# Kernel tuning notes

Hardware: AMD Instinct MI355X
Metric: run time of the kernel (lower is better)

Reference implementation:

```python
import jax, jax.numpy as jnp
import numpy as np

NUM_CLASSES = 2
NORM_EPS = 1e-12   # F.normalize default
COS_EPS = 1e-8     # nn.CosineSimilarity default
MEAN_EPS = 1e-6


def _l2_normalize_c(x):
    # normalize over channel dim (dim=1), per (batch, pixel) -- matches
    # F.normalize(x.view(-1,16,256*256), dim=1)
    n = jnp.sqrt(jnp.sum(x * x, axis=1, keepdims=True))
    return x / jnp.maximum(n, NORM_EPS)


def _cos_c(a, b):
    # cosine similarity along channel dim, torch semantics
    dot = jnp.sum(a * b, axis=1)
    na = jnp.sqrt(jnp.sum(a * a, axis=1))
    nb = jnp.sqrt(jnp.sum(b * b, axis=1))
    return dot / jnp.maximum(na * nb, COS_EPS)


def setup_inputs() -> dict:
    key = jax.random.key(0)
    k1, k2, k3 = jax.random.split(key, 3)
    preds_S = jax.random.normal(k1, (32, 16, 256, 256), dtype=jnp.float32)
    preds_T = jax.random.normal(k2, (32, 16, 256, 256), dtype=jnp.float32)
    target = jax.random.randint(k3, (32, 256, 256), 0, NUM_CLASSES, dtype=jnp.int64)
    return {"preds_S": preds_S, "preds_T": preds_T, "target": target}


def reference(preds_S, preds_T, target):
    feat_S = _l2_normalize_c(preds_S)  # [B,16,H,W]
    feat_T = _l2_normalize_c(preds_T)
    # target is already HxW == feature size, so nearest upsample is identity
    tar = target[:, None, :, :].astype(feat_S.dtype)  # [B,1,H,W], broadcasts over C

    center_S, center_T = feat_S, feat_T
    center_S_FS, center_T_FS = feat_S, feat_T
    for i in range(NUM_CLASSES):
        mask = (tar == i).astype(feat_S.dtype)  # [B,1,H,W]
        cnt = jnp.sum(mask, axis=(-2, -1)) + MEAN_EPS  # [B,1]
        mean_S = (jnp.sum(mask * feat_S, axis=(-2, -1)) / cnt)[:, :, None, None]  # [B,16,1,1]
        mean_T = (jnp.sum(mask * feat_T, axis=(-2, -1)) / cnt)[:, :, None, None]
        center_S = (1.0 - mask) * center_S + mask * mean_S
        center_T = (1.0 - mask) * center_T + mask * mean_T
        center_S_FS = mask * center_S_FS + (1.0 - mask) * mean_S
        center_T_FS = mask * center_T_FS + (1.0 - mask) * mean_T

    pcsim_S = jnp.exp(_cos_c(feat_S, center_S) - _cos_c(feat_S, center_S_FS))
    pcsim_T = jnp.exp(_cos_c(feat_T, center_T) - _cos_c(feat_T, center_T_FS))
    return jnp.mean((pcsim_S - pcsim_T) ** 2)
```

## Files before the change

### kernel.cpp

```cpp
#include <hip/hip_runtime.h>
#include <math.h>

#define NBATCH 32
#define NCH 16
#define HW 65536
#define SLICES1 32
#define SLICES2 32
#define TPB 256

#define CT_PART  0
#define CT_N1P   65536
#define CT_LOSSP 66560
#define CT_FLOATS 67584

#define CACHE_HALFS ((size_t)2 * NBATCH * NCH * HW)
#define CACHE_BYTES (CACHE_HALFS * 2)

typedef float f4 __attribute__((ext_vector_type(4)));
typedef _Float16 h4 __attribute__((ext_vector_type(4)));
typedef _Float16 h8 __attribute__((ext_vector_type(8)));

__device__ __forceinline__ float wave_sum(float v) {
#pragma unroll
  for (int off = 32; off > 0; off >>= 1) v += __shfl_down(v, off, 64);
  return v;
}

template <bool CACHE>
__global__ __launch_bounds__(TPB) void k_sums(const float* __restrict__ S,
                                              const float* __restrict__ T,
                                              const int* __restrict__ tgt,
                                              float* __restrict__ ctrl,
                                              _Float16* __restrict__ cache) {
  const int b = blockIdx.y;
  const int slice = blockIdx.x;
  const int which = blockIdx.z;
  const int tid = threadIdx.x;
  const int lane = tid & 63, wid = tid >> 6;

  const float* Xb = (which ? T : S) + (size_t)b * NCH * HW;
  const int* tb = tgt + (size_t)b * HW;
  _Float16* cb = cache + ((size_t)(which * NBATCH + b)) * NCH * HW;

  const int base = slice * (HW / SLICES1) + tid * 4;

  float acc0[NCH], acc1[NCH];
#pragma unroll
  for (int i = 0; i < NCH; ++i) { acc0[i] = 0.f; acc1[i] = 0.f; }
  float n1 = 0.f;

  for (int it = 0; it < 2; ++it) {
    const int p = base + it * (TPB * 4);
    const int4 tv = *(const int4*)(tb + p);
    f4 x[NCH];
#pragma unroll
    for (int i = 0; i < NCH; ++i)
      x[i] = __builtin_nontemporal_load((const f4*)(Xb + (size_t)i * HW + p));

    const float m0 = (tv.x == 1) ? 1.f : 0.f;
    const float m1 = (tv.y == 1) ? 1.f : 0.f;
    const float m2 = (tv.z == 1) ? 1.f : 0.f;
    const float m3 = (tv.w == 1) ? 1.f : 0.f;
    n1 += (m0 + m1) + (m2 + m3);

    float s0a = 0.f, s0b = 0.f, s1a = 0.f, s1b = 0.f;
    float s2a = 0.f, s2b = 0.f, s3a = 0.f, s3b = 0.f;
#pragma unroll
    for (int i = 0; i < NCH; i += 2) {
      s0a = fmaf(x[i].x, x[i].x, s0a);   s0b = fmaf(x[i + 1].x, x[i + 1].x, s0b);
      s1a = fmaf(x[i].y, x[i].y, s1a);   s1b = fmaf(x[i + 1].y, x[i + 1].y, s1b);
      s2a = fmaf(x[i].z, x[i].z, s2a);   s2b = fmaf(x[i + 1].z, x[i + 1].z, s2b);
      s3a = fmaf(x[i].w, x[i].w, s3a);   s3b = fmaf(x[i + 1].w, x[i + 1].w, s3b);
    }
    const float i0 = 1.f / fmaxf(sqrtf(s0a + s0b), 1e-12f);
    const float i1 = 1.f / fmaxf(sqrtf(s1a + s1b), 1e-12f);
    const float i2 = 1.f / fmaxf(sqrtf(s2a + s2b), 1e-12f);
    const float i3 = 1.f / fmaxf(sqrtf(s3a + s3b), 1e-12f);

#pragma unroll
    for (int i = 0; i < NCH; ++i) {
      const float f0 = x[i].x * i0, f1 = x[i].y * i1;
      const float f2 = x[i].z * i2, f3 = x[i].w * i3;
      if constexpr (CACHE) {
        h4 q;
        q.x = (_Float16)f0; q.y = (_Float16)f1;
        q.z = (_Float16)f2; q.w = (_Float16)f3;
        __builtin_nontemporal_store(q, (h4*)(cb + (size_t)i * HW + p));
      }
      const float t_ = (f0 + f1) + (f2 + f3);
      const float m_ = fmaf(f0, m0, fmaf(f1, m1, fmaf(f2, m2, f3 * m3)));
      acc1[i] += m_;
      acc0[i] += t_ - m_;
    }
  }

  __shared__ float lds[32][TPB + 1];
  __shared__ float redn[4];
#pragma unroll
  for (int i = 0; i < NCH; ++i) {
    lds[i][tid] = acc0[i];
    lds[16 + i][tid] = acc1[i];
  }
  n1 = wave_sum(n1);
  if (lane == 0) redn[wid] = n1;
  __syncthreads();

  const int row = tid >> 3, seg = tid & 7;
  float s = 0.f;
#pragma unroll
  for (int k0 = 0; k0 < 32; ++k0) {
    const int k = (k0 + seg * 4) & 31;
    s += lds[row][seg * 32 + k];
  }
  s += __shfl_down(s, 4, 8);
  s += __shfl_down(s, 2, 8);
  s += __shfl_down(s, 1, 8);

  float* part = ctrl + CT_PART + (((size_t)which * NBATCH + b) * SLICES1 + slice) * 32;
  if (seg == 0) part[row] = s;
  if (tid == 0 && which == 0)
    ctrl[CT_N1P + b * SLICES1 + slice] = redn[0] + redn[1] + redn[2] + redn[3];
}

__device__ __forceinline__ float pc_one(float ss, float d0, float d1, int t,
                                        float nm0, float nm1) {
  const float n = sqrtf(ss);
  const float inv = 1.f / fmaxf(n, 1e-12f);
  const float na = n * inv;
  const float c0 = (d0 * inv) / fmaxf(na * nm0, 1e-8f);
  const float c1 = (d1 * inv) / fmaxf(na * nm1, 1e-8f);
  return expf((t == 1) ? (c1 - c0) : (c0 - c1));
}

template <bool CACHE>
__global__ __launch_bounds__(TPB) void k_pass2(const float* __restrict__ S,
                                               const float* __restrict__ T,
                                               const int* __restrict__ tgt,
                                               float* __restrict__ ctrl,
                                               const _Float16* __restrict__ cache) {
  __shared__ __align__(16) float sm[72];
  __shared__ float ldp[4][64];
  __shared__ float ldn[32];
  __shared__ float red4[4];
  const int b = blockIdx.y;
  const int slice = blockIdx.x;
  const int tid = threadIdx.x;

  {
    const int c64 = tid & 63, q = tid >> 6;
    const int t_ = c64 >> 5, c32 = c64 & 31;
    const float* pp = ctrl + CT_PART + (((size_t)t_ * NBATCH + b) * SLICES1) * 32 + c32;
    float s8 = 0.f;
#pragma unroll
    for (int k = 0; k < 8; ++k) s8 += pp[(q * 8 + k) * 32];
    ldp[q][c64] = s8;
  }
  if (tid < 32) ldn[tid] = ctrl[CT_N1P + b * SLICES1 + tid];
  __syncthreads();

  if (tid < 64) {
    float n1 = 0.f;
#pragma unroll
    for (int k = 0; k < 32; ++k) n1 += ldn[k];
    const int cls = (tid >> 4) & 1;
    const float cnt = (cls ? n1 : ((float)HW - n1)) + 1e-6f;
    sm[tid] = (ldp[0][tid] + ldp[1][tid] + ldp[2][tid] + ldp[3][tid]) / cnt;
  }
  __syncthreads();
  if (tid < 4) {
    float ss = 0.f;
    const int base_ = (tid >> 1) * 32 + (tid & 1) * 16;
#pragma unroll
    for (int c = 0; c < NCH; ++c) { const float v = sm[base_ + c]; ss = fmaf(v, v, ss); }
    sm[64 + tid] = sqrtf(ss);
  }
  __syncthreads();

  const int* tb = tgt + (size_t)b * HW;
  float lacc = 0.f;

  if constexpr (CACHE) {
    const _Float16* cS = cache + (size_t)b * NCH * HW;
    const _Float16* cT = cache + ((size_t)(NBATCH + b)) * NCH * HW;
    const float rS0 = 1.f / fmaxf(sm[64], 1e-8f);
    const float rS1 = 1.f / fmaxf(sm[65], 1e-8f);
    const float rT0 = 1.f / fmaxf(sm[66], 1e-8f);
    const float rT1 = 1.f / fmaxf(sm[67], 1e-8f);

    const int p = slice * (HW / SLICES2) + tid * 8;
    const int4 tva = *(const int4*)(tb + p);
    const int4 tvb = *(const int4*)(tb + p + 4);
    const int t8[8] = {tva.x, tva.y, tva.z, tva.w, tvb.x, tvb.y, tvb.z, tvb.w};

    h8 xs[NCH], xt[NCH];
#pragma unroll
    for (int i = 0; i < NCH; ++i)
      xs[i] = __builtin_nontemporal_load((const h8*)(cS + (size_t)i * HW + p));
#pragma unroll
    for (int i = 0; i < NCH; ++i)
      xt[i] = __builtin_nontemporal_load((const h8*)(cT + (size_t)i * HW + p));

    float a0[8], a1[8];
#pragma unroll
    for (int k = 0; k < 8; ++k) { a0[k] = 0.f; a1[k] = 0.f; }
#pragma unroll
    for (int i = 0; i < NCH; ++i) {
      const float w0 = sm[i], w1 = sm[16 + i];
#pragma unroll
      for (int k = 0; k < 8; ++k) {
        const float xv = (float)xs[i][k];
        a0[k] = fmaf(xv, w0, a0[k]);
        a1[k] = fmaf(xv, w1, a1[k]);
      }
    }
    float pcS[8];
#pragma unroll
    for (int k = 0; k < 8; ++k)
      pcS[k] = expf((t8[k] == 1) ? a1[k] * rS1 - a0[k] * rS0
                                 : a0[k] * rS0 - a1[k] * rS1);

#pragma unroll
    for (int k = 0; k < 8; ++k) { a0[k] = 0.f; a1[k] = 0.f; }
#pragma unroll
    for (int i = 0; i < NCH; ++i) {
      const float w0 = sm[32 + i], w1 = sm[48 + i];
#pragma unroll
      for (int k = 0; k < 8; ++k) {
        const float xv = (float)xt[i][k];
        a0[k] = fmaf(xv, w0, a0[k]);
        a1[k] = fmaf(xv, w1, a1[k]);
      }
    }
#pragma unroll
    for (int k = 0; k < 8; ++k) {
      const float pcT = expf((t8[k] == 1) ? a1[k] * rT1 - a0[k] * rT0
                                          : a0[k] * rT0 - a1[k] * rT1);
      const float e = pcS[k] - pcT;
      lacc = fmaf(e, e, lacc);
    }
  } else {
    const float* Sb = S + (size_t)b * NCH * HW;
    const float* Tb = T + (size_t)b * NCH * HW;
    const float nmS0 = sm[64], nmS1 = sm[65], nmT0 = sm[66], nmT1 = sm[67];
    const int base = slice * (HW / SLICES2) + tid * 2;

    for (int it = 0; it < 4; ++it) {
      const int p = base + it * (TPB * 2);
      const int2 tv = *(const int2*)(tb + p);
      float2 xs[NCH], xt[NCH];
#pragma unroll
      for (int i = 0; i < NCH; ++i) xs[i] = *(const float2*)(Sb + (size_t)i * HW + p);
#pragma unroll
      for (int i = 0; i < NCH; ++i) xt[i] = *(const float2*)(Tb + (size_t)i * HW + p);

      float ss0 = 0.f, ss1 = 0.f, d00 = 0.f, d01 = 0.f, d10 = 0.f, d11 = 0.f;
#pragma unroll
      for (int i = 0; i < NCH; ++i) {
        const float w0 = sm[i], w1 = sm[16 + i];
        ss0 = fmaf(xs[i].x, xs[i].x, ss0); ss1 = fmaf(xs[i].y, xs[i].y, ss1);
        d00 = fmaf(xs[i].x, w0, d00);      d01 = fmaf(xs[i].y, w0, d01);
        d10 = fmaf(xs[i].x, w1, d10);      d11 = fmaf(xs[i].y, w1, d11);
      }
      const float pcS0 = pc_one(ss0, d00, d10, tv.x, nmS0, nmS1);
      const float pcS1 = pc_one(ss1, d01, d11, tv.y, nmS0, nmS1);

      ss0 = 0.f; ss1 = 0.f; d00 = 0.f; d01 = 0.f; d10 = 0.f; d11 = 0.f;
#pragma unroll
      for (int i = 0; i < NCH; ++i) {
        const float w0 = sm[32 + i], w1 = sm[48 + i];
        ss0 = fmaf(xt[i].x, xt[i].x, ss0); ss1 = fmaf(xt[i].y, xt[i].y, ss1);
        d00 = fmaf(xt[i].x, w0, d00);      d01 = fmaf(xt[i].y, w0, d01);
        d10 = fmaf(xt[i].x, w1, d10);      d11 = fmaf(xt[i].y, w1, d11);
      }
      const float pcT0 = pc_one(ss0, d00, d10, tv.x, nmT0, nmT1);
      const float pcT1 = pc_one(ss1, d01, d11, tv.y, nmT0, nmT1);

      const float e0 = pcS0 - pcT0, e1 = pcS1 - pcT1;
      lacc += e0 * e0 + e1 * e1;
    }
  }

  lacc = wave_sum(lacc);
  if ((tid & 63) == 0) red4[tid >> 6] = lacc;
  __syncthreads();
  if (tid == 0)
    ctrl[CT_LOSSP + b * SLICES2 + slice] = red4[0] + red4[1] + red4[2] + red4[3];
}

__global__ void k_final(const float* __restrict__ ctrl, float* __restrict__ out) {
  __shared__ float r4[4];
  const int tid = threadIdx.x;
  float s = ctrl[CT_LOSSP + tid] + ctrl[CT_LOSSP + tid + 256] +
            ctrl[CT_LOSSP + tid + 512] + ctrl[CT_LOSSP + tid + 768];
  s = wave_sum(s);
  if ((tid & 63) == 0) r4[tid >> 6] = s;
  __syncthreads();
  if (tid == 0)
    out[0] = (r4[0] + r4[1] + r4[2] + r4[3]) * (1.f / 2097152.f);
}

extern "C" void kernel_launch(void* const* d_in, const int* in_sizes, int n_in,
                              void* d_out, int out_size, void* d_ws, size_t ws_size,
                              hipStream_t stream) {
  const float* S = (const float*)d_in[0];
  const float* T = (const float*)d_in[1];
  const int* tgt = (const int*)d_in[2];
  float* out = (float*)d_out;

  const size_t need = CACHE_BYTES + (size_t)CT_FLOATS * 4;
  const bool cached = ws_size >= need;
  _Float16* cache = (_Float16*)d_ws;
  float* ctrl = cached ? (float*)((char*)d_ws + CACHE_BYTES) : (float*)d_ws;

  dim3 g1(SLICES1, NBATCH, 2);
  dim3 g2(SLICES2, NBATCH);
  if (cached) {
    k_sums<true><<<g1, TPB, 0, stream>>>(S, T, tgt, ctrl, cache);
    k_pass2<true><<<g2, TPB, 0, stream>>>(S, T, tgt, ctrl, cache);
  } else {
    k_sums<false><<<g1, TPB, 0, stream>>>(S, T, tgt, ctrl, cache);
    k_pass2<false><<<g2, TPB, 0, stream>>>(S, T, tgt, ctrl, cache);
  }
  k_final<<<1, 256, 0, stream>>>(ctrl, out);
}
```

Measured before the change: 312.8 us.

## Fuse three kernels into one cooperative persistent kernel with grid syncs

Replaces the sums/pass2/final kernel sequence with a single cooperative launch of 512 persistent blocks that loop over work units and separate the stages with grid-wide barriers, removing two launch gaps and the tails between kernels. It also adds an occupancy hint to the fallback pass2 kernel. In exchange, each stage is confined to a fixed grid with two blocks per CU, which caps the loads in flight, and grid syncs add their own cost. The old multi-kernel path is kept only as a fallback if the cooperative launch fails.

After: 454.4 us. 1.45x slower.

```diff
diff --git a/kernel.cpp b/kernel.cpp
--- a/kernel.cpp
+++ b/kernel.cpp
@@ -1,5 +1,8 @@
 #include <hip/hip_runtime.h>
+#include <hip/hip_cooperative_groups.h>
 #include <math.h>
+
+namespace cg = cooperative_groups;
 
 #define NBATCH 32
 #define NCH 16
@@ -7,6 +10,7 @@
 #define SLICES1 32
 #define SLICES2 32
 #define TPB 256
+#define COOP_GRID 512
 
 #define CT_PART  0
 #define CT_N1P   65536
@@ -24,6 +28,219 @@
 #pragma unroll
   for (int off = 32; off > 0; off >>= 1) v += __shfl_down(v, off, 64);
   return v;
+}
+
+__global__ __launch_bounds__(TPB, 2) void k_fused(const float* __restrict__ S,
+                                                  const float* __restrict__ T,
+                                                  const int* __restrict__ tgt,
+                                                  float* __restrict__ ctrl,
+                                                  _Float16* __restrict__ cache,
+                                                  float* __restrict__ out) {
+  cg::grid_group gg = cg::this_grid();
+  __shared__ float lds[32][TPB + 1];
+  __shared__ float redn[4];
+  __shared__ __align__(16) float sm[72];
+  __shared__ float ldp[4][64];
+  __shared__ float ldn[32];
+  __shared__ float red4[4];
+  const int tid = threadIdx.x;
+  const int lane = tid & 63, wid = tid >> 6;
+
+  for (int u = blockIdx.x; u < 2 * NBATCH * SLICES1; u += COOP_GRID) {
+    const int which = u >> 10;
+    const int b = (u >> 5) & 31;
+    const int slice = u & 31;
+    const float* Xb = (which ? T : S) + (size_t)b * NCH * HW;
+    const int* tb = tgt + (size_t)b * HW;
+    _Float16* cb = cache + ((size_t)(which * NBATCH + b)) * NCH * HW;
+    const int base = slice * (HW / SLICES1) + tid * 4;
+
+    float acc0[NCH], acc1[NCH];
+#pragma unroll
+    for (int i = 0; i < NCH; ++i) { acc0[i] = 0.f; acc1[i] = 0.f; }
+    float n1 = 0.f;
+
+    for (int it = 0; it < 2; ++it) {
+      const int p = base + it * (TPB * 4);
+      const int4 tv = *(const int4*)(tb + p);
+      f4 x[NCH];
+#pragma unroll
+      for (int i = 0; i < NCH; ++i)
+        x[i] = __builtin_nontemporal_load((const f4*)(Xb + (size_t)i * HW + p));
+
+      const float m0 = (tv.x == 1) ? 1.f : 0.f;
+      const float m1 = (tv.y == 1) ? 1.f : 0.f;
+      const float m2 = (tv.z == 1) ? 1.f : 0.f;
+      const float m3 = (tv.w == 1) ? 1.f : 0.f;
+      const float g0 = 1.f - 2.f * m0, g1 = 1.f - 2.f * m1;
+      const float g2 = 1.f - 2.f * m2, g3 = 1.f - 2.f * m3;
+      n1 += (m0 + m1) + (m2 + m3);
+
+      float s0a = 0.f, s0b = 0.f, s1a = 0.f, s1b = 0.f;
+      float s2a = 0.f, s2b = 0.f, s3a = 0.f, s3b = 0.f;
+#pragma unroll
+      for (int i = 0; i < NCH; i += 2) {
+        s0a = fmaf(x[i].x, x[i].x, s0a);   s0b = fmaf(x[i + 1].x, x[i + 1].x, s0b);
+        s1a = fmaf(x[i].y, x[i].y, s1a);   s1b = fmaf(x[i + 1].y, x[i + 1].y, s1b);
+        s2a = fmaf(x[i].z, x[i].z, s2a);   s2b = fmaf(x[i + 1].z, x[i + 1].z, s2b);
+        s3a = fmaf(x[i].w, x[i].w, s3a);   s3b = fmaf(x[i + 1].w, x[i + 1].w, s3b);
+      }
+      const float i0 = 1.f / fmaxf(sqrtf(s0a + s0b), 1e-12f);
+      const float i1 = 1.f / fmaxf(sqrtf(s1a + s1b), 1e-12f);
+      const float i2 = 1.f / fmaxf(sqrtf(s2a + s2b), 1e-12f);
+      const float i3 = 1.f / fmaxf(sqrtf(s3a + s3b), 1e-12f);
+
+#pragma unroll
+      for (int i = 0; i < NCH; ++i) {
+        const float f0 = x[i].x * i0, f1 = x[i].y * i1;
+        const float f2 = x[i].z * i2, f3 = x[i].w * i3;
+        h4 q;
+        q.x = (_Float16)(f0 * g0); q.y = (_Float16)(f1 * g1);
+        q.z = (_Float16)(f2 * g2); q.w = (_Float16)(f3 * g3);
+        __builtin_nontemporal_store(q, (h4*)(cb + (size_t)i * HW + p));
+        const float t_ = (f0 + f1) + (f2 + f3);
+        const float m_ = fmaf(f0, m0, fmaf(f1, m1, fmaf(f2, m2, f3 * m3)));
+        acc1[i] += m_;
+        acc0[i] += t_ - m_;
+      }
+    }
+
+    __syncthreads();
+#pragma unroll
+    for (int i = 0; i < NCH; ++i) {
+      lds[i][tid] = acc0[i];
+      lds[16 + i][tid] = acc1[i];
+    }
+    n1 = wave_sum(n1);
+    if (lane == 0) redn[wid] = n1;
+    __syncthreads();
+
+    const int row = tid >> 3, seg = tid & 7;
+    float s = 0.f;
+#pragma unroll
+    for (int k0 = 0; k0 < 32; ++k0) {
+      const int k = (k0 + seg * 4) & 31;
+      s += lds[row][seg * 32 + k];
+    }
+    s += __shfl_down(s, 4, 8);
+    s += __shfl_down(s, 2, 8);
+    s += __shfl_down(s, 1, 8);
+
+    float* part = ctrl + CT_PART + (((size_t)which * NBATCH + b) * SLICES1 + slice) * 32;
+    if (seg == 0) part[row] = s;
+    if (tid == 0 && which == 0)
+      ctrl[CT_N1P + b * SLICES1 + slice] = redn[0] + redn[1] + redn[2] + redn[3];
+  }
+
+  gg.sync();
+
+  for (int u = blockIdx.x; u < NBATCH * SLICES2; u += COOP_GRID) {
+    const int b = u >> 5, slice = u & 31;
+    __syncthreads();
+
+    {
+      const int c64 = tid & 63, q = tid >> 6;
+      const int t_ = c64 >> 5, c32 = c64 & 31;
+      const float* pp = ctrl + CT_PART + (((size_t)t_ * NBATCH + b) * SLICES1) * 32 + c32;
+      float s8 = 0.f;
+#pragma unroll
+      for (int k = 0; k < 8; ++k) s8 += pp[(q * 8 + k) * 32];
+      ldp[q][c64] = s8;
+    }
+    if (tid < 32) ldn[tid] = ctrl[CT_N1P + b * SLICES1 + tid];
+    __syncthreads();
+
+    if (tid < 64) {
+      float n1 = 0.f;
+#pragma unroll
+      for (int k = 0; k < 32; ++k) n1 += ldn[k];
+      const int cls = (tid >> 4) & 1;
+      const float cnt = (cls ? n1 : ((float)HW - n1)) + 1e-6f;
+      sm[tid] = (ldp[0][tid] + ldp[1][tid] + ldp[2][tid] + ldp[3][tid]) / cnt;
+    }
+    __syncthreads();
+    if (tid < 4) {
+      float ss = 0.f;
+      const int base_ = (tid >> 1) * 32 + (tid & 1) * 16;
+#pragma unroll
+      for (int c = 0; c < NCH; ++c) { const float v = sm[base_ + c]; ss = fmaf(v, v, ss); }
+      sm[64 + tid] = sqrtf(ss);
+    }
+    __syncthreads();
+
+    const _Float16* cS = cache + (size_t)b * NCH * HW;
+    const _Float16* cT = cache + ((size_t)(NBATCH + b)) * NCH * HW;
+    const float rS0 = 1.f / fmaxf(sm[64], 1e-8f);
+    const float rS1 = 1.f / fmaxf(sm[65], 1e-8f);
+    const float rT0 = 1.f / fmaxf(sm[66], 1e-8f);
+    const float rT1 = 1.f / fmaxf(sm[67], 1e-8f);
+
+    const int p = slice * (HW / SLICES2) + tid * 8;
+
+    h8 xs[NCH], xt[NCH];
+#pragma unroll
+    for (int i = 0; i < NCH; ++i)
+      xs[i] = __builtin_nontemporal_load((const h8*)(cS + (size_t)i * HW + p));
+#pragma unroll
+    for (int i = 0; i < NCH; ++i)
+      xt[i] = __builtin_nontemporal_load((const h8*)(cT + (size_t)i * HW + p));
+
+    float a0S[8], a1S[8];
+#pragma unroll
+    for (int k = 0; k < 8; ++k) { a0S[k] = 0.f; a1S[k] = 0.f; }
+#pragma unroll
+    for (int i = 0; i < NCH; ++i) {
+      const float w0 = sm[i], w1 = sm[16 + i];
+#pragma unroll
+      for (int k = 0; k < 8; ++k) {
+        const float xv = (float)xs[i][k];
+        a0S[k] = fmaf(xv, w0, a0S[k]);
+        a1S[k] = fmaf(xv, w1, a1S[k]);
+      }
+    }
+    float pcS[8];
+#pragma unroll
+    for (int k = 0; k < 8; ++k) pcS[k] = expf(a0S[k] * rS0 - a1S[k] * rS1);
+
+    float a0T[8], a1T[8];
+#pragma unroll
+    for (int k = 0; k < 8; ++k) { a0T[k] = 0.f; a1T[k] = 0.f; }
+#pragma unroll
+    for (int i = 0; i < NCH; ++i) {
+      const float w0 = sm[32 + i], w1 = sm[48 + i];
+#pragma unroll
+      for (int k = 0; k < 8; ++k) {
+        const float xv = (float)xt[i][k];
+        a0T[k] = fmaf(xv, w0, a0T[k]);
+        a1T[k] = fmaf(xv, w1, a1T[k]);
+      }
+    }
+    float lacc = 0.f;
+#pragma unroll
+    for (int k = 0; k < 8; ++k) {
+      const float pcT = expf(a0T[k] * rT0 - a1T[k] * rT1);
+      const float e = pcS[k] - pcT;
+      lacc = fmaf(e, e, lacc);
+    }
+
+    lacc = wave_sum(lacc);
+    if ((tid & 63) == 0) red4[tid >> 6] = lacc;
+    __syncthreads();
+    if (tid == 0)
+      ctrl[CT_LOSSP + u] = red4[0] + red4[1] + red4[2] + red4[3];
+  }
+
+  gg.sync();
+
+  if (blockIdx.x == 0) {
+    float s = ctrl[CT_LOSSP + tid] + ctrl[CT_LOSSP + tid + 256] +
+              ctrl[CT_LOSSP + tid + 512] + ctrl[CT_LOSSP + tid + 768];
+    s = wave_sum(s);
+    if ((tid & 63) == 0) red4[tid >> 6] = s;
+    __syncthreads();
+    if (tid == 0)
+      out[0] = (red4[0] + red4[1] + red4[2] + red4[3]) * (1.f / 2097152.f);
+  }
 }
 
 template <bool CACHE>
@@ -41,7 +258,6 @@
   const float* Xb = (which ? T : S) + (size_t)b * NCH * HW;
   const int* tb = tgt + (size_t)b * HW;
   _Float16* cb = cache + ((size_t)(which * NBATCH + b)) * NCH * HW;
-
   const int base = slice * (HW / SLICES1) + tid * 4;
 
   float acc0[NCH], acc1[NCH];
@@ -133,11 +349,11 @@
 }
 
 template <bool CACHE>
-__global__ __launch_bounds__(TPB) void k_pass2(const float* __restrict__ S,
-                                               const float* __restrict__ T,
-                                               const int* __restrict__ tgt,
-                                               float* __restrict__ ctrl,
-                                               const _Float16* __restrict__ cache) {
+__global__ __launch_bounds__(TPB, 3) void k_pass2(const float* __restrict__ S,
+                                                  const float* __restrict__ T,
+                                                  const int* __restrict__ tgt,
+                                                  float* __restrict__ ctrl,
+                                                  const _Float16* __restrict__ cache) {
   __shared__ __align__(16) float sm[72];
   __shared__ float ldp[4][64];
   __shared__ float ldn[32];
@@ -312,6 +528,14 @@
   _Float16* cache = (_Float16*)d_ws;
   float* ctrl = cached ? (float*)((char*)d_ws + CACHE_BYTES) : (float*)d_ws;
 
+  if (cached) {
+    void* args[] = {(void*)&S, (void*)&T, (void*)&tgt,
+                    (void*)&ctrl, (void*)&cache, (void*)&out};
+    const hipError_t e = hipLaunchCooperativeKernel(
+        (const void*)k_fused, dim3(COOP_GRID), dim3(TPB), args, 0, stream);
+    if (e == hipSuccess) return;
+  }
+
   dim3 g1(SLICES1, NBATCH, 2);
   dim3 g2(SLICES2, NBATCH);
   if (cached) {
```
